# Kernel tuning notes

Measured on AMD Instinct MI355X. Metric: run time of the kernel, lower is better.

Reference implementation:

```python
import jax, jax.numpy as jnp
import numpy as np

DECAY = 0.999
EPS = 1e-05
COMMIT = 0.25


def _layer_norm(x, g, b, eps=1e-5):
    mu = x.mean(-1, keepdims=True)
    var = ((x - mu) ** 2).mean(-1, keepdims=True)
    return (x - mu) * jax.lax.rsqrt(var + eps) * g + b


def setup_inputs() -> dict:
    key = jax.random.key(0)
    ks = jax.random.split(key, 8)
    B, T, D, M, H = 8, 4096, 512, 1024, 512
    init_bound = 1.0 / 512
    embedding = jax.random.uniform(ks[0], (M, D), jnp.float32, -init_bound, init_bound)
    return {
        "dense_x": jax.random.normal(ks[1], (B, T, D), jnp.float32),
        "dense_padding_mask": jax.random.randint(ks[2], (B, T), 0, 2).astype(bool),
        "labels": jax.random.randint(ks[3], (B, T), 0, M),
        "embedding": embedding,
        "ema_count": jnp.zeros((M,), jnp.float32),
        "ema_weight": embedding,
        "ln1_g": jnp.ones((D,), jnp.float32),
        "ln1_b": jnp.zeros((D,), jnp.float32),
        "W1": jax.random.normal(ks[4], (D, H), jnp.float32) * (1.0 / np.sqrt(D)),
        "ln2_g": jnp.ones((H,), jnp.float32),
        "ln2_b": jnp.zeros((H,), jnp.float32),
        "W2": jax.random.normal(ks[5], (H, M), jnp.float32) * (1.0 / np.sqrt(H)),
    }


def reference(dense_x, dense_padding_mask, labels, embedding, ema_count, ema_weight,
              ln1_g, ln1_b, W1, ln2_g, ln2_b, W2):
    B, T, D = dense_x.shape
    M = embedding.shape[0]
    N = B * T

    # ---- VQ codebook (EMA) ----
    x_flat = jax.lax.stop_gradient(dense_x).reshape(N, D)
    distances = (jnp.sum(embedding ** 2, axis=1)[None, :]
                 + jnp.sum(x_flat ** 2, axis=1, keepdims=True)
                 - 2.0 * (x_flat @ embedding.T))
    indices = jnp.argmin(distances, axis=-1)  # [N]
    quantized = embedding[indices].reshape(B, T, D)

    # EMA codebook update (training path); encodings.sum(0) and encodings.T @ x
    # expressed as scatter-adds instead of materializing [N, M] one-hot.
    counts = jnp.zeros((M,), dense_x.dtype).at[indices].add(1.0)
    new_count = DECAY * ema_count + (1.0 - DECAY) * counts
    n = jnp.sum(new_count)
    new_count = (new_count + EPS) / (n + M * EPS) * n
    dw = jnp.zeros((M, D), dense_x.dtype).at[indices].add(x_flat)
    new_weight = DECAY * ema_weight + (1.0 - DECAY) * dw
    new_embedding = new_weight / new_count[:, None]

    e_latent_loss = (dense_x - jax.lax.stop_gradient(quantized)) ** 2  # [B,T,D]
    vq_loss = COMMIT * e_latent_loss
    quantized_st = dense_x + jax.lax.stop_gradient(quantized - dense_x)

    avg_probs = counts / N
    perplexity = jnp.exp(-jnp.sum(avg_probs * jnp.log(avg_probs + 1e-10)))

    # ---- decoder: LN -> ReLU -> Linear -> LN -> ReLU -> Linear ----
    h = jax.nn.relu(_layer_norm(dense_x, ln1_g, ln1_b)) @ W1      # [B,T,H]
    logits = jax.nn.relu(_layer_norm(h, ln2_g, ln2_b)) @ W2       # [B,T,M]

    # ---- cross-entropy with ignore_index=-1 (padding) ----
    lab = jnp.where(dense_padding_mask, -1, labels)
    valid = lab >= 0
    safe = jnp.where(valid, lab, 0)
    logp = jax.nn.log_softmax(logits, axis=-1)
    ce = -jnp.take_along_axis(logp, safe[..., None], axis=-1)[..., 0]
    recon_loss = jnp.where(valid, ce, 0.0)

    loss = recon_loss + vq_loss.sum(-1)  # [B,T]
    return quantized_st, loss, perplexity, new_embedding, new_count, new_weight
```

## Files before the change

kernel.cpp:

```cpp
#include <hip/hip_runtime.h>


#define N_TOK 32768
#define WAITV(n) __builtin_amdgcn_s_waitcnt(0x0F70 | (n))
#define BAR() __builtin_amdgcn_s_barrier()

typedef __attribute__((ext_vector_type(8))) short short8;
typedef _Float16 half8 __attribute__((ext_vector_type(8)));
typedef __attribute__((ext_vector_type(4))) float f32x4;

__device__ __forceinline__ f32x4 mfma16(short8 a, short8 b, f32x4 c) {
    return __builtin_amdgcn_mfma_f32_16x16x32_bf16(a, b, c, 0, 0, 0);
}
__device__ __forceinline__ f32x4 mfma16h(half8 a, half8 b, f32x4 c) {
    return __builtin_amdgcn_mfma_f32_16x16x32_f16(a, b, c, 0, 0, 0);
}

__device__ __forceinline__ void gl_lds16(const unsigned short* g, char* l) {
    __builtin_amdgcn_global_load_lds(
        (const __attribute__((address_space(1))) void*)g,
        (__attribute__((address_space(3))) void*)l, 16, 0, 0);
}

__device__ __forceinline__ unsigned short f2bf(float x) {
    unsigned u = __float_as_uint(x);
    u += 0x7fffu + ((u >> 16) & 1u);
    return (unsigned short)(u >> 16);
}
__device__ __forceinline__ float bf2f(unsigned short h) {
    return __uint_as_float(((unsigned)h) << 16);
}
__device__ __forceinline__ unsigned short f2h(float x) {
    union { _Float16 h; unsigned short u; } c;
    c.h = (_Float16)x;
    return c.u;
}
__device__ __forceinline__ float h2f(unsigned short u) {
    union { _Float16 h; unsigned short u; } c;
    c.u = u;
    return (float)c.h;
}

__device__ __forceinline__ float waveSum(float v) {
#pragma unroll
    for (int off = 32; off > 0; off >>= 1) v += __shfl_down(v, off, 64);
    return v;
}
__device__ __forceinline__ float xorSum(float v) {
#pragma unroll
    for (int off = 1; off < 64; off <<= 1) v += __shfl_xor(v, off);
    return v;
}

__global__ __launch_bounds__(256) void prep_x_kernel(
        const float* __restrict__ X, const float* __restrict__ g,
        const float* __restrict__ b, unsigned short* __restrict__ Xf,
        unsigned short* __restrict__ A1, unsigned long long* __restrict__ minpack) {
    int tid = threadIdx.x;
    if (tid < 4) minpack[(blockIdx.x << 2) + tid] = ~0ULL;
    int lane = tid & 63;
    int n = (blockIdx.x << 2) + (tid >> 6);
    const float* row = X + ((size_t)n << 9);
    float v[8]; float s = 0.f, ss = 0.f;
#pragma unroll
    for (int i = 0; i < 8; ++i) { v[i] = row[lane + (i << 6)]; s += v[i]; ss += v[i] * v[i]; }
    s = xorSum(s); ss = xorSum(ss);
    float mu = s * (1.f / 512.f);
    float rs = rsqrtf(ss * (1.f / 512.f) - mu * mu + 1e-5f);
#pragma unroll
    for (int i = 0; i < 8; ++i) {
        int c = lane + (i << 6);
        size_t o = ((size_t)n << 9) + c;
        float x = v[i];
        Xf[o] = f2h(x);
        float a = fmaxf((x - mu) * rs * g[c] + b[c], 0.f);
        A1[o] = f2bf(a);
    }
}

__global__ __launch_bounds__(256) void prep_e_kernel(
        const float* __restrict__ E, unsigned short* __restrict__ Ehf,
        unsigned short* __restrict__ Elf, float* __restrict__ e_sq,
        int* __restrict__ izero) {
    if (blockIdx.x < 8) izero[(blockIdx.x << 8) + threadIdx.x] = 0;
    int lane = threadIdx.x & 63;
    int m = (blockIdx.x << 2) + (threadIdx.x >> 6);
    const float* row = E + ((size_t)m << 9);
    float ss = 0.f;
#pragma unroll
    for (int i = 0; i < 8; ++i) {
        int c = lane + (i << 6);
        float x = row[c];
        ss += x * x;
        float xs = x * 512.f;
        unsigned short h = f2h(xs);
        size_t o = ((size_t)m << 9) + c;
        Ehf[o] = h;
        Elf[o] = f2h(xs - h2f(h));
    }
    ss = xorSum(ss);
    if (lane == 0) e_sq[m] = ss * 512.f;
}

__global__ __launch_bounds__(256) void prep_wt_kernel(
        const float* __restrict__ W1, const float* __restrict__ W2,
        unsigned short* __restrict__ W1T, unsigned short* __restrict__ W2T) {
    __shared__ float t[32][33];
    int bx = blockIdx.x;
    const float* W = (bx < 16) ? W1 : W2;
    unsigned short* WT = (bx < 16) ? W1T : W2T;
    int Nw = (bx < 16) ? 512 : 1024;
    int n0 = ((bx < 16) ? bx : (bx - 16)) << 5, k0 = blockIdx.y << 5;
    int tx = threadIdx.x & 31, ty = threadIdx.x >> 5;
#pragma unroll
    for (int l = 0; l < 4; ++l)
        t[ty + (l << 3)][tx] = W[(size_t)(k0 + ty + (l << 3)) * Nw + n0 + tx];
    __syncthreads();
#pragma unroll
    for (int l = 0; l < 4; ++l)
        WT[(((size_t)(n0 + ty + (l << 3))) << 9) + k0 + tx] = f2bf(t[tx][ty + (l << 3)]);
}

__device__ __forceinline__ unsigned long long packDist(float d, int m) {
    unsigned u = __float_as_uint(d);
    u = (u & 0x80000000u) ? ~u : (u | 0x80000000u);
    return ((unsigned long long)u << 32) | (unsigned)m;
}

__device__ __forceinline__ void dist_body(
        int q, int x, char* LB,
        const unsigned short* __restrict__ Xf,
        const unsigned short* __restrict__ Ehf, const unsigned short* __restrict__ Elf,
        const float* __restrict__ e_sq, unsigned long long* __restrict__ minpack) {
    int tid = threadIdx.x, lane = tid & 63, w = tid >> 6;
    int quad = lane >> 4, lanelo = lane & 15;
    int wm = w >> 1, wn = w & 1;
    int row0 = (((q >> 3) << 3) | x) << 7;
    int m0 = (q & 7) << 7;

    int srow = ((w & 1) << 6) + lane;
    int skoff = (w >> 1) << 4;
    const unsigned short* pX = Xf  + (((size_t)(row0 + srow)) << 9) + skoff;
    const unsigned short* pH = Ehf + (((size_t)(m0  + srow)) << 9) + skoff;
    const unsigned short* pL = Elf + (((size_t)(m0  + srow)) << 9) + skoff;
    char* ldsB = LB + ((w >> 1) << 12) + ((w & 1) << 10) + (lane << 4);
    const char* ra  = LB + (quad << 11) + (((wm << 6) + lanelo) << 4);
    const char* rbh = LB + 8192 + (quad << 11) + (((wn << 6) + lanelo) << 4);

    f32x4 acc[4][4];
#pragma unroll
    for (int i = 0; i < 4; ++i)
#pragma unroll
        for (int j = 0; j < 4; ++j) acc[i][j] = 0.f;

#pragma unroll
    for (int p = 0; p < 2; ++p) {
        char* d = ldsB + p * 24576;
        const unsigned short* sX = pX + (p << 5);
        const unsigned short* sH = pH + (p << 5);
        const unsigned short* sL = pL + (p << 5);
        gl_lds16(sX, d);            gl_lds16(sX + 8, d + 2048);
        gl_lds16(sH, d + 8192);     gl_lds16(sH + 8, d + 10240);
        gl_lds16(sL, d + 16384);    gl_lds16(sL + 8, d + 18432);
    }

#pragma unroll
    for (int it = 0; it < 16; ++it) {
        const int cb = it % 3;
        if (it < 14) {
            const int nb = (it + 2) % 3;
            const unsigned short* sX = pX + ((it + 2) << 5);
            const unsigned short* sH = pH + ((it + 2) << 5);
            const unsigned short* sL = pL + ((it + 2) << 5);
            char* d = ldsB + nb * 24576;
            gl_lds16(sX, d);            gl_lds16(sX + 8, d + 2048);
            gl_lds16(sH, d + 8192);     gl_lds16(sH + 8, d + 10240);
            gl_lds16(sL, d + 16384);    gl_lds16(sL + 8, d + 18432);
            WAITV(12);
        } else if (it == 14) {
            WAITV(6);
        } else {
            WAITV(0);
        }
        BAR();
        const char* A  = ra  + cb * 24576;
        const char* Bh = rbh + cb * 24576;
        half8 av[4], bh[4], bl[4];
#pragma unroll
        for (int i = 0; i < 4; ++i) av[i] = *(const half8*)(A + (i << 8));
#pragma unroll
        for (int j = 0; j < 4; ++j) {
            bh[j] = *(const half8*)(Bh + (j << 8));
            bl[j] = *(const half8*)(Bh + 8192 + (j << 8));
        }
#pragma unroll
        for (int i = 0; i < 4; ++i)
#pragma unroll
            for (int j = 0; j < 4; ++j) acc[i][j] = mfma16h(av[i], bh[j], acc[i][j]);
#pragma unroll
        for (int i = 0; i < 4; ++i)
#pragma unroll
            for (int j = 0; j < 4; ++j) acc[i][j] = mfma16h(av[i], bl[j], acc[i][j]);
        BAR();
    }

    float esq[4];
#pragma unroll
    for (int j = 0; j < 4; ++j) esq[j] = e_sq[m0 + (wn << 6) + (j << 4) + lanelo];
#pragma unroll
    for (int i = 0; i < 4; ++i)
#pragma unroll
        for (int r = 0; r < 4; ++r) {
            unsigned long long best = ~0ULL;
#pragma unroll
            for (int j = 0; j < 4; ++j) {
                int code = m0 + (wn << 6) + (j << 4) + lanelo;
                float d = esq[j] - 2.f * acc[i][j][r];
                unsigned long long p = packDist(d, code);
                if (p < best) best = p;
            }
#pragma unroll
            for (int off = 1; off < 16; off <<= 1) {
                unsigned long long q2 = __shfl_xor(best, off);
                if (q2 < best) best = q2;
            }
            if (lanelo == 0) {
                int t = row0 + (wm << 6) + (i << 4) + (quad << 2) + r;
                atomicMin(&minpack[t], best);
            }
        }
}

__device__ __forceinline__ void gemm_core(
        char* LB, const unsigned short* pA, const unsigned short* pB,
        int w, int lane, int quad, int lanelo, int wm, int wn,
        f32x4 (*acc)[4], bool bf) {
    char* ldsB = LB + ((w >> 1) << 12) + ((w & 1) << 10) + (lane << 4);
    const char* ra = LB + (quad << 11) + (((wm << 6) + lanelo) << 4);
    const char* rb = LB + 8192 + (quad << 11) + (((wn << 6) + lanelo) << 4);

#pragma unroll
    for (int p = 0; p < 2; ++p) {
        char* d = ldsB + p * 16384;
        const unsigned short* sA = pA + (p << 5);
        const unsigned short* sB = pB + (p << 5);
        gl_lds16(sA, d);            gl_lds16(sA + 8, d + 2048);
        gl_lds16(sB, d + 8192);     gl_lds16(sB + 8, d + 10240);
    }

#pragma unroll
    for (int it = 0; it < 16; ++it) {
        const int cb = it % 3;
        if (it < 14) {
            const int nb = (it + 2) % 3;
            const unsigned short* sA = pA + ((it + 2) << 5);
            const unsigned short* sB = pB + ((it + 2) << 5);
            char* d = ldsB + nb * 16384;
            gl_lds16(sA, d);            gl_lds16(sA + 8, d + 2048);
            gl_lds16(sB, d + 8192);     gl_lds16(sB + 8, d + 10240);
            WAITV(8);
        } else if (it == 14) {
            WAITV(4);
        } else {
            WAITV(0);
        }
        BAR();
        const char* A = ra + cb * 16384;
        const char* B = rb + cb * 16384;
        short8 af[4], bf4[4];
#pragma unroll
        for (int i = 0; i < 4; ++i) af[i] = *(const short8*)(A + (i << 8));
#pragma unroll
        for (int j = 0; j < 4; ++j) bf4[j] = *(const short8*)(B + (j << 8));
#pragma unroll
        for (int i = 0; i < 4; ++i)
#pragma unroll
            for (int j = 0; j < 4; ++j) acc[i][j] = mfma16(af[i], bf4[j], acc[i][j]);
        BAR();
    }
    (void)bf;
}

__device__ __forceinline__ void gemm1_body(
        int g, int x, char* LB,
        const unsigned short* __restrict__ A1, const unsigned short* __restrict__ W1T,
        unsigned short* __restrict__ Hb) {
    int tid = threadIdx.x, lane = tid & 63, w = tid >> 6;
    int quad = lane >> 4, lanelo = lane & 15;
    int wm = w >> 1, wn = w & 1;
    int row0 = (((g >> 2) << 3) | x) << 7;
    int n0 = (g & 3) << 7;

    int srow = ((w & 1) << 6) + lane;
    int skoff = (w >> 1) << 4;
    const unsigned short* pA = A1  + (((size_t)(row0 + srow)) << 9) + skoff;
    const unsigned short* pB = W1T + (((size_t)(n0   + srow)) << 9) + skoff;

    f32x4 acc[4][4];
#pragma unroll
    for (int i = 0; i < 4; ++i)
#pragma unroll
        for (int j = 0; j < 4; ++j) acc[i][j] = 0.f;

    gemm_core(LB, pA, pB, w, lane, quad, lanelo, wm, wn, acc, true);

#pragma unroll
    for (int i = 0; i < 4; ++i)
#pragma unroll
        for (int j = 0; j < 4; ++j)
#pragma unroll
            for (int r = 0; r < 4; ++r) {
                int row = row0 + (wm << 6) + (i << 4) + (quad << 2) + r;
                int col = n0 + (wn << 6) + (j << 4) + lanelo;
                Hb[((size_t)row << 9) + col] = f2bf(acc[i][j][r]);
            }
}

__global__ __launch_bounds__(256) void fused1_kernel(
        const unsigned short* __restrict__ Xf,
        const unsigned short* __restrict__ Ehf, const unsigned short* __restrict__ Elf,
        const float* __restrict__ e_sq, unsigned long long* __restrict__ minpack,
        const unsigned short* __restrict__ A1, const unsigned short* __restrict__ W1T,
        unsigned short* __restrict__ Hb) {
    __shared__ __align__(16) char LB[73728];
    int b = blockIdx.x, x = b & 7, m = b >> 3;
    int t = m % 3, g = m / 3;
    if (t < 2) dist_body((g << 1) + t, x, LB, Xf, Ehf, Elf, e_sq, minpack);
    else       gemm1_body(g, x, LB, A1, W1T, Hb);
}

__global__ __launch_bounds__(256) void fused2_kernel(
        const float* __restrict__ X, const float* __restrict__ E,
        const unsigned long long* __restrict__ minpack,
        float* __restrict__ out_q, int* __restrict__ icounts,
        float* __restrict__ vqsum,
        const unsigned short* __restrict__ Hb, const float* __restrict__ g2,
        const float* __restrict__ b2, unsigned short* __restrict__ A2) {
    int nb = blockIdx.x >> 1;
    int lane = threadIdx.x & 63;
    int n = (nb << 2) + (threadIdx.x >> 6);
    if ((blockIdx.x & 1) == 0) {
        int idx = (int)(minpack[n] & 0xFFFFFFFFULL);
        if (lane == 0) atomicAdd(&icounts[idx], 1);
        const float* xr = X + ((size_t)n << 9);
        const float* er = E + ((size_t)idx << 9);
        float s = 0.f;
#pragma unroll
        for (int i = 0; i < 8; ++i) {
            int c = lane + (i << 6);
            float xv = xr[c], q = er[c];
            out_q[((size_t)n << 9) + c] = q;
            float dlt = xv - q;
            s += dlt * dlt;
        }
        s = waveSum(s);
        if (lane == 0) vqsum[n] = 0.25f * s;
    } else {
        const unsigned short* row = Hb + ((size_t)n << 9);
        float v[8]; float s = 0.f, ss = 0.f;
#pragma unroll
        for (int i = 0; i < 8; ++i) { v[i] = bf2f(row[lane + (i << 6)]); s += v[i]; ss += v[i] * v[i]; }
        s = xorSum(s); ss = xorSum(ss);
        float mu = s * (1.f / 512.f);
        float rs = rsqrtf(ss * (1.f / 512.f) - mu * mu + 1e-5f);
#pragma unroll
        for (int i = 0; i < 8; ++i) {
            int c = lane + (i << 6);
            float a = fmaxf((v[i] - mu) * rs * g2[c] + b2[c], 0.f);
            A2[((size_t)n << 9) + c] = f2bf(a);
        }
    }
}

__global__ __launch_bounds__(1024) void codebook_kernel(
        const float* __restrict__ ema_count, const int* __restrict__ icounts,
        float* __restrict__ out_perp, float* __restrict__ out_newcount,
        int* __restrict__ offsets) {
    __shared__ int sc[1024];
    __shared__ float red[16];
    int tid = threadIdx.x;
    int lane = tid & 63, wid = tid >> 6;
    int ic = icounts[tid];
    sc[tid] = ic;
    for (int off = 1; off < 1024; off <<= 1) {
        __syncthreads();
        int v = (tid >= off) ? sc[tid - off] : 0;
        __syncthreads();
        sc[tid] += v;
    }
    offsets[tid] = sc[tid] - ic;
    __syncthreads();

    float cnt = (float)ic;
    float raw = 0.999f * ema_count[tid] + 0.001f * cnt;
    float v = waveSum(raw);
    if (lane == 0) red[wid] = v;
    __syncthreads();
    float nsum = 0.f;
#pragma unroll
    for (int i = 0; i < 16; ++i) nsum += red[i];
    __syncthreads();
    float p = cnt * (1.f / 32768.f);
    float e = p * logf(p + 1e-10f);
    e = waveSum(e);
    if (lane == 0) red[wid] = e;
    __syncthreads();
    float ent = 0.f;
#pragma unroll
    for (int i = 0; i < 16; ++i) ent += red[i];
    float nc = (raw + 1e-5f) / (nsum + 1024.f * 1e-5f) * nsum;
    out_newcount[tid] = nc;
    if (tid == 0) out_perp[0] = expf(-ent);
}

__global__ __launch_bounds__(256) void scatter_kernel(
        const unsigned long long* __restrict__ minpack,
        const int* __restrict__ offsets, int* __restrict__ cursor,
        int* __restrict__ bucket) {
    int n = (blockIdx.x << 8) + threadIdx.x;
    int idx = (int)(minpack[n] & 0xFFFFFFFFULL);
    int pos = atomicAdd(&cursor[idx], 1);
    bucket[offsets[idx] + pos] = n;
}

__device__ __forceinline__ void dw_body(
        int m, char* LB, const float* __restrict__ X,
        const int* __restrict__ bucket, const int* __restrict__ icounts,
        const int* __restrict__ offsets, float* __restrict__ dw) {
    float* comb = (float*)LB;
    int tid = threadIdx.x, lane = tid & 63, w = tid >> 6;
    int cnt = icounts[m], base = offsets[m];
    float acc[8] = {};
    for (int i = w; i < cnt; i += 4) {
        int t = bucket[base + i];
        const float* xr = X + ((size_t)t << 9);
#pragma unroll
        for (int j = 0; j < 8; ++j) acc[j] += xr[lane + (j << 6)];
    }
#pragma unroll
    for (int j = 0; j < 8; ++j) comb[(w << 9) + lane + (j << 6)] = acc[j];
    __syncthreads();
    for (int c = tid; c < 512; c += 256)
        dw[((size_t)m << 9) + c] = comb[c] + comb[512 + c] + comb[1024 + c] + comb[1536 + c];
}

__device__ __forceinline__ void gemm2_body(
        int q, int x, char* LB,
        float (*lmax)[2][64], float (*lsum)[2][64], float* llab, int* slab,
        const unsigned short* __restrict__ A2, const unsigned short* __restrict__ W2T,
        const int* __restrict__ mask, const int* __restrict__ labels,
        float* __restrict__ ws_cmax, float* __restrict__ ws_csum,
        float* __restrict__ ws_lab) {
    int tid = threadIdx.x, lane = tid & 63, w = tid >> 6;
    int quad = lane >> 4, lanelo = lane & 15;
    int wm = w >> 1, wn = w & 1;
    int row0 = (((q >> 3) << 3) | x) << 7;
    int cy = q & 7;
    int c0 = cy << 7;
    if (tid < 128) {
        int mk = mask[row0 + tid];
        slab[tid] = mk ? 0 : labels[row0 + tid];
    }
    __syncthreads();

    int srow = ((w & 1) << 6) + lane;
    int skoff = (w >> 1) << 4;
    const unsigned short* pA = A2  + (((size_t)(row0 + srow)) << 9) + skoff;
    const unsigned short* pB = W2T + (((size_t)(c0   + srow)) << 9) + skoff;

    f32x4 acc[4][4];
#pragma unroll
    for (int i = 0; i < 4; ++i)
#pragma unroll
        for (int j = 0; j < 4; ++j) acc[i][j] = 0.f;

    gemm_core(LB, pA, pB, w, lane, quad, lanelo, wm, wn, acc, true);

#pragma unroll
    for (int i = 0; i < 4; ++i)
#pragma unroll
        for (int j = 0; j < 4; ++j)
#pragma unroll
            for (int r = 0; r < 4; ++r) {
                int code = c0 + (wn << 6) + (j << 4) + lanelo;
                int tt = (wm << 6) + (i << 4) + (quad << 2) + r;
                if (code == slab[tt]) llab[tt] = acc[i][j][r];
            }
#pragma unroll
    for (int i = 0; i < 4; ++i)
#pragma unroll
        for (int r = 0; r < 4; ++r) {
            float mx = fmaxf(fmaxf(acc[i][0][r], acc[i][1][r]),
                             fmaxf(acc[i][2][r], acc[i][3][r]));
#pragma unroll
            for (int off = 1; off < 16; off <<= 1) mx = fmaxf(mx, __shfl_xor(mx, off));
            if (lanelo == 0) lmax[wm][wn][(i << 4) + (quad << 2) + r] = mx;
        }
    __syncthreads();
#pragma unroll
    for (int i = 0; i < 4; ++i)
#pragma unroll
        for (int r = 0; r < 4; ++r) {
            int tl = (i << 4) + (quad << 2) + r;
            float cm = fmaxf(lmax[wm][0][tl], lmax[wm][1][tl]);
            float s2 = expf(acc[i][0][r] - cm) + expf(acc[i][1][r] - cm) +
                       expf(acc[i][2][r] - cm) + expf(acc[i][3][r] - cm);
#pragma unroll
            for (int off = 1; off < 16; off <<= 1) s2 += __shfl_xor(s2, off);
            if (lanelo == 0) lsum[wm][wn][tl] = s2;
        }
    __syncthreads();
    if (tid < 128) {
        int wmi = tid >> 6, tl = tid & 63;
        int token = row0 + tid;
        float cm = fmaxf(lmax[wmi][0][tl], lmax[wmi][1][tl]);
        float cs = lsum[wmi][0][tl] + lsum[wmi][1][tl];
        size_t o = ((size_t)cy << 15) + token;
        ws_cmax[o] = cm;
        ws_csum[o] = cs;
        if ((slab[tid] >> 7) == cy) ws_lab[token] = llab[tid];
    }
}

__global__ __launch_bounds__(256) void fused3_kernel(
        const unsigned short* __restrict__ A2, const unsigned short* __restrict__ W2T,
        const int* __restrict__ mask, const int* __restrict__ labels,
        float* __restrict__ ws_cmax, float* __restrict__ ws_csum,
        float* __restrict__ ws_lab,
        const float* __restrict__ X, const int* __restrict__ bucket,
        const int* __restrict__ icounts, const int* __restrict__ offsets,
        float* __restrict__ dw) {
    __shared__ __align__(16) char LB[49152];
    __shared__ float lmax[2][2][64], lsum[2][2][64], llab[128];
    __shared__ int slab[128];
    int b = blockIdx.x, x = b & 7, m = b >> 3;
    int t = m % 3, g = m / 3;
    if (t < 2) gemm2_body((g << 1) + t, x, LB, lmax, lsum, llab, slab,
                          A2, W2T, mask, labels, ws_cmax, ws_csum, ws_lab);
    else       dw_body((g << 3) | x, LB, X, bucket, icounts, offsets, dw);
}

__global__ __launch_bounds__(256) void epilogue_kernel(
        const float* __restrict__ ema_weight, const float* __restrict__ dw,
        const float* __restrict__ newcount, float* __restrict__ out_neww,
        float* __restrict__ out_newemb,
        const float* __restrict__ ws_cmax, const float* __restrict__ ws_csum,
        const float* __restrict__ ws_lab, const int* __restrict__ mask,
        const float* __restrict__ vqsum, float* __restrict__ loss_out) {
    int bx = blockIdx.x;
    if (bx < 2048) {
        int i = (bx << 8) + threadIdx.x;
        float nw = 0.999f * ema_weight[i] + 0.001f * dw[i];
        out_neww[i] = nw;
        out_newemb[i] = nw / newcount[i >> 9];
    } else {
        int n = ((bx - 2048) << 8) + threadIdx.x;
        float m[8], s[8];
#pragma unroll
        for (int c = 0; c < 8; ++c) {
            m[c] = ws_cmax[(c << 15) + n];
            s[c] = ws_csum[(c << 15) + n];
        }
        float gm = m[0];
#pragma unroll
        for (int c = 1; c < 8; ++c) gm = fmaxf(gm, m[c]);
        float se = 0.f;
#pragma unroll
        for (int c = 0; c < 8; ++c) se += s[c] * expf(m[c] - gm);
        float ce = -(ws_lab[n] - gm - logf(se));
        loss_out[n] = (mask[n] ? 0.f : ce) + vqsum[n];
    }
}

extern "C" void kernel_launch(void* const* d_in, const int* in_sizes, int n_in,
                              void* d_out, int out_size, void* d_ws, size_t ws_size,
                              hipStream_t stream) {
    const float* X          = (const float*)d_in[0];
    const int*   mask       = (const int*)d_in[1];
    const int*   labels     = (const int*)d_in[2];
    const float* E          = (const float*)d_in[3];
    const float* ema_count  = (const float*)d_in[4];
    const float* ema_weight = (const float*)d_in[5];
    const float* g1 = (const float*)d_in[6];
    const float* b1 = (const float*)d_in[7];
    const float* W1 = (const float*)d_in[8];
    const float* g2 = (const float*)d_in[9];
    const float* b2 = (const float*)d_in[10];
    const float* W2 = (const float*)d_in[11];

    float* out = (float*)d_out;
    float* out_q        = out;
    float* out_loss     = out + 16777216;
    float* out_perp     = out + 16809984;
    float* out_newemb   = out + 16809985;
    float* out_newcount = out + 17334273;
    float* out_neww     = out + 17335297;

    float* w = (float*)d_ws;
    float* vqsum = w;  w += 32768;
    float* e_sq = w;   w += 1024;
    float* dwbuf = w;  w += 524288;
    unsigned long long* minpack = (unsigned long long*)w; w += 65536;
    float* ws_cmax = w; w += 262144;
    float* ws_csum = w; w += 262144;
    float* ws_lab  = w; w += 32768;
    int* icounts = (int*)w; w += 1024;
    int* cursor  = (int*)w; w += 1024;
    int* offsets = (int*)w; w += 1024;
    int* bucket  = (int*)w; w += 32768;
    unsigned short* Ehf = (unsigned short*)w; w += 262144;
    unsigned short* Elf = (unsigned short*)w; w += 262144;
    unsigned short* W1T = (unsigned short*)w; w += 131072;
    unsigned short* W2T = (unsigned short*)w; w += 262144;
    unsigned short* Xf  = (unsigned short*)w; w += 8388608;
    unsigned short* A1  = (unsigned short*)w; w += 8388608;
    unsigned short* Hb  = (unsigned short*)w; w += 8388608;
    unsigned short* A2  = Xf;

    prep_e_kernel<<<256, 256, 0, stream>>>(E, Ehf, Elf, e_sq, icounts);
    prep_wt_kernel<<<dim3(48, 16), 256, 0, stream>>>(W1, W2, W1T, W2T);
    prep_x_kernel<<<8192, 256, 0, stream>>>(X, g1, b1, Xf, A1, minpack);
    fused1_kernel<<<3072, 256, 0, stream>>>(Xf, Ehf, Elf, e_sq, minpack,
                                            A1, W1T, Hb);
    fused2_kernel<<<16384, 256, 0, stream>>>(X, E, minpack, out_q, icounts,
                                             vqsum, Hb, g2, b2, A2);
    codebook_kernel<<<1, 1024, 0, stream>>>(ema_count, icounts, out_perp,
                                            out_newcount, offsets);
    scatter_kernel<<<128, 256, 0, stream>>>(minpack, offsets, cursor, bucket);
    fused3_kernel<<<3072, 256, 0, stream>>>(A2, W2T, mask, labels,
                                            ws_cmax, ws_csum, ws_lab,
                                            X, bucket, icounts, offsets, dwbuf);
    epilogue_kernel<<<2176, 256, 0, stream>>>(ema_weight, dwbuf, out_newcount,
                                              out_neww, out_newemb,
                                              ws_cmax, ws_csum, ws_lab,
                                              mask, vqsum, out_loss);
}
```

Baseline: 481.4 us.

## Enlarge GEMM tiles to 256 rows with 512-thread blocks and double buffering

The distance, GEMM1 and GEMM2 bodies now use 512-thread blocks, each covering 256 token rows instead of 128, so every codebook or weight tile loaded into LDS is reused across twice as many rows. The three-stage LDS ring becomes two-stage double buffering to fit the larger tiles, and grids are halved to match. The dw body is widened to use eight waves, and the fused3 block mapping changes so GEMM2 and dw blocks alternate. The trade-offs are a shallower prefetch pipeline, higher LDS use per block and fewer resident blocks, which may expose more memory latency.

```diff
diff --git a/kernel.cpp b/kernel.cpp
--- a/kernel.cpp
+++ b/kernel.cpp
@@ -135,17 +135,18 @@
     int tid = threadIdx.x, lane = tid & 63, w = tid >> 6;
     int quad = lane >> 4, lanelo = lane & 15;
     int wm = w >> 1, wn = w & 1;
-    int row0 = (((q >> 3) << 3) | x) << 7;
+    int row0 = (((q >> 3) << 3) | x) << 8;
     int m0 = (q & 7) << 7;
 
-    int srow = ((w & 1) << 6) + lane;
-    int skoff = (w >> 1) << 4;
-    const unsigned short* pX = Xf  + (((size_t)(row0 + srow)) << 9) + skoff;
-    const unsigned short* pH = Ehf + (((size_t)(m0  + srow)) << 9) + skoff;
-    const unsigned short* pL = Elf + (((size_t)(m0  + srow)) << 9) + skoff;
-    char* ldsB = LB + ((w >> 1) << 12) + ((w & 1) << 10) + (lane << 4);
-    const char* ra  = LB + (quad << 11) + (((wm << 6) + lanelo) << 4);
-    const char* rbh = LB + 8192 + (quad << 11) + (((wn << 6) + lanelo) << 4);
+    int mA = tid & 255, kA = tid >> 8;
+    int nB = tid & 127, kB = tid >> 7;
+    const unsigned short* pA = Xf  + (((size_t)(row0 + mA)) << 9) + (kA << 3);
+    const unsigned short* pH = Ehf + (((size_t)(m0  + nB)) << 9) + (kB << 3);
+    const unsigned short* pL = Elf + (((size_t)(m0  + nB)) << 9) + (kB << 3);
+    char* dA = LB + (tid << 4);
+    char* dB = LB + 16384 + (tid << 4);
+    const char* ra  = LB + (quad << 12) + (((wm << 6) + lanelo) << 4);
+    const char* rbh = LB + 16384 + (quad << 11) + (((wn << 6) + lanelo) << 4);
 
     f32x4 acc[4][4];
 #pragma unroll
@@ -153,38 +154,27 @@
 #pragma unroll
         for (int j = 0; j < 4; ++j) acc[i][j] = 0.f;
 
-#pragma unroll
-    for (int p = 0; p < 2; ++p) {
-        char* d = ldsB + p * 24576;
-        const unsigned short* sX = pX + (p << 5);
-        const unsigned short* sH = pH + (p << 5);
-        const unsigned short* sL = pL + (p << 5);
-        gl_lds16(sX, d);            gl_lds16(sX + 8, d + 2048);
-        gl_lds16(sH, d + 8192);     gl_lds16(sH + 8, d + 10240);
-        gl_lds16(sL, d + 16384);    gl_lds16(sL + 8, d + 18432);
-    }
+    gl_lds16(pA, dA);   gl_lds16(pA + 16, dA + 8192);
+    gl_lds16(pH, dB);   gl_lds16(pL, dB + 8192);
 
 #pragma unroll
     for (int it = 0; it < 16; ++it) {
-        const int cb = it % 3;
-        if (it < 14) {
-            const int nb = (it + 2) % 3;
-            const unsigned short* sX = pX + ((it + 2) << 5);
-            const unsigned short* sH = pH + ((it + 2) << 5);
-            const unsigned short* sL = pL + ((it + 2) << 5);
-            char* d = ldsB + nb * 24576;
-            gl_lds16(sX, d);            gl_lds16(sX + 8, d + 2048);
-            gl_lds16(sH, d + 8192);     gl_lds16(sH + 8, d + 10240);
-            gl_lds16(sL, d + 16384);    gl_lds16(sL + 8, d + 18432);
-            WAITV(12);
-        } else if (it == 14) {
-            WAITV(6);
+        const int cb = it & 1;
+        if (it < 15) {
+            const unsigned short* sA = pA + ((it + 1) << 5);
+            const unsigned short* sH = pH + ((it + 1) << 5);
+            const unsigned short* sL = pL + ((it + 1) << 5);
+            char* eA = dA + (cb ^ 1) * 32768;
+            char* eB = dB + (cb ^ 1) * 32768;
+            gl_lds16(sA, eA);   gl_lds16(sA + 16, eA + 8192);
+            gl_lds16(sH, eB);   gl_lds16(sL, eB + 8192);
+            WAITV(4);
         } else {
             WAITV(0);
         }
         BAR();
-        const char* A  = ra  + cb * 24576;
-        const char* Bh = rbh + cb * 24576;
+        const char* A  = ra  + cb * 32768;
+        const char* Bh = rbh + cb * 32768;
         half8 av[4], bh[4], bl[4];
 #pragma unroll
         for (int i = 0; i < 4; ++i) av[i] = *(const half8*)(A + (i << 8));
@@ -231,42 +221,37 @@
         }
 }
 
-__device__ __forceinline__ void gemm_core(
+__device__ __forceinline__ void gemm_core512(
         char* LB, const unsigned short* pA, const unsigned short* pB,
-        int w, int lane, int quad, int lanelo, int wm, int wn,
-        f32x4 (*acc)[4], bool bf) {
-    char* ldsB = LB + ((w >> 1) << 12) + ((w & 1) << 10) + (lane << 4);
-    const char* ra = LB + (quad << 11) + (((wm << 6) + lanelo) << 4);
-    const char* rb = LB + 8192 + (quad << 11) + (((wn << 6) + lanelo) << 4);
-
-#pragma unroll
-    for (int p = 0; p < 2; ++p) {
-        char* d = ldsB + p * 16384;
-        const unsigned short* sA = pA + (p << 5);
-        const unsigned short* sB = pB + (p << 5);
-        gl_lds16(sA, d);            gl_lds16(sA + 8, d + 2048);
-        gl_lds16(sB, d + 8192);     gl_lds16(sB + 8, d + 10240);
-    }
+        f32x4 (*acc)[4]) {
+    int tid = threadIdx.x, lane = tid & 63, w = tid >> 6;
+    int quad = lane >> 4, lanelo = lane & 15;
+    int wm = w >> 1, wn = w & 1;
+    char* dA = LB + (tid << 4);
+    char* dB = LB + 16384 + (tid << 4);
+    const char* ra = LB + (quad << 12) + (((wm << 6) + lanelo) << 4);
+    const char* rb = LB + 16384 + (quad << 11) + (((wn << 6) + lanelo) << 4);
+
+    gl_lds16(pA, dA);   gl_lds16(pA + 16, dA + 8192);
+    gl_lds16(pB, dB);
 
 #pragma unroll
     for (int it = 0; it < 16; ++it) {
-        const int cb = it % 3;
-        if (it < 14) {
-            const int nb = (it + 2) % 3;
-            const unsigned short* sA = pA + ((it + 2) << 5);
-            const unsigned short* sB = pB + ((it + 2) << 5);
-            char* d = ldsB + nb * 16384;
-            gl_lds16(sA, d);            gl_lds16(sA + 8, d + 2048);
-            gl_lds16(sB, d + 8192);     gl_lds16(sB + 8, d + 10240);
-            WAITV(8);
-        } else if (it == 14) {
-            WAITV(4);
+        const int cb = it & 1;
+        if (it < 15) {
+            const unsigned short* sA = pA + ((it + 1) << 5);
+            const unsigned short* sB = pB + ((it + 1) << 5);
+            char* eA = dA + (cb ^ 1) * 24576;
+            char* eB = dB + (cb ^ 1) * 24576;
+            gl_lds16(sA, eA);   gl_lds16(sA + 16, eA + 8192);
+            gl_lds16(sB, eB);
+            WAITV(3);
         } else {
             WAITV(0);
         }
         BAR();
-        const char* A = ra + cb * 16384;
-        const char* B = rb + cb * 16384;
+        const char* A = ra + cb * 24576;
+        const char* B = rb + cb * 24576;
         short8 af[4], bf4[4];
 #pragma unroll
         for (int i = 0; i < 4; ++i) af[i] = *(const short8*)(A + (i << 8));
@@ -278,7 +263,6 @@
             for (int j = 0; j < 4; ++j) acc[i][j] = mfma16(af[i], bf4[j], acc[i][j]);
         BAR();
     }
-    (void)bf;
 }
 
 __device__ __forceinline__ void gemm1_body(
@@ -288,13 +272,13 @@
     int tid = threadIdx.x, lane = tid & 63, w = tid >> 6;
     int quad = lane >> 4, lanelo = lane & 15;
     int wm = w >> 1, wn = w & 1;
-    int row0 = (((g >> 2) << 3) | x) << 7;
+    int row0 = (((g >> 2) << 3) | x) << 8;
     int n0 = (g & 3) << 7;
 
-    int srow = ((w & 1) << 6) + lane;
-    int skoff = (w >> 1) << 4;
-    const unsigned short* pA = A1  + (((size_t)(row0 + srow)) << 9) + skoff;
-    const unsigned short* pB = W1T + (((size_t)(n0   + srow)) << 9) + skoff;
+    int mA = tid & 255, kA = tid >> 8;
+    int nB = tid & 127, kB = tid >> 7;
+    const unsigned short* pA = A1  + (((size_t)(row0 + mA)) << 9) + (kA << 3);
+    const unsigned short* pB = W1T + (((size_t)(n0   + nB)) << 9) + (kB << 3);
 
     f32x4 acc[4][4];
 #pragma unroll
@@ -302,7 +286,7 @@
 #pragma unroll
         for (int j = 0; j < 4; ++j) acc[i][j] = 0.f;
 
-    gemm_core(LB, pA, pB, w, lane, quad, lanelo, wm, wn, acc, true);
+    gemm_core512(LB, pA, pB, acc);
 
 #pragma unroll
     for (int i = 0; i < 4; ++i)
@@ -316,13 +300,13 @@
             }
 }
 
-__global__ __launch_bounds__(256) void fused1_kernel(
+__global__ __launch_bounds__(512) void fused1_kernel(
         const unsigned short* __restrict__ Xf,
         const unsigned short* __restrict__ Ehf, const unsigned short* __restrict__ Elf,
         const float* __restrict__ e_sq, unsigned long long* __restrict__ minpack,
         const unsigned short* __restrict__ A1, const unsigned short* __restrict__ W1T,
         unsigned short* __restrict__ Hb) {
-    __shared__ __align__(16) char LB[73728];
+    __shared__ __align__(16) char LB[65536];
     int b = blockIdx.x, x = b & 7, m = b >> 3;
     int t = m % 3, g = m / 3;
     if (t < 2) dist_body((g << 1) + t, x, LB, Xf, Ehf, Elf, e_sq, minpack);
@@ -431,7 +415,7 @@
     int tid = threadIdx.x, lane = tid & 63, w = tid >> 6;
     int cnt = icounts[m], base = offsets[m];
     float acc[8] = {};
-    for (int i = w; i < cnt; i += 4) {
+    for (int i = w; i < cnt; i += 8) {
         int t = bucket[base + i];
         const float* xr = X + ((size_t)t << 9);
 #pragma unroll
@@ -440,8 +424,13 @@
 #pragma unroll
     for (int j = 0; j < 8; ++j) comb[(w << 9) + lane + (j << 6)] = acc[j];
     __syncthreads();
-    for (int c = tid; c < 512; c += 256)
-        dw[((size_t)m << 9) + c] = comb[c] + comb[512 + c] + comb[1024 + c] + comb[1536 + c];
+    int c = tid;
+    if (c < 512) {
+        float s = 0.f;
+#pragma unroll
+        for (int p = 0; p < 8; ++p) s += comb[(p << 9) + c];
+        dw[((size_t)m << 9) + c] = s;
+    }
 }
 
 __device__ __forceinline__ void gemm2_body(
@@ -454,19 +443,19 @@
     int tid = threadIdx.x, lane = tid & 63, w = tid >> 6;
     int quad = lane >> 4, lanelo = lane & 15;
     int wm = w >> 1, wn = w & 1;
-    int row0 = (((q >> 3) << 3) | x) << 7;
+    int row0 = (((q >> 3) << 3) | x) << 8;
     int cy = q & 7;
     int c0 = cy << 7;
-    if (tid < 128) {
+    if (tid < 256) {
         int mk = mask[row0 + tid];
         slab[tid] = mk ? 0 : labels[row0 + tid];
     }
     __syncthreads();
 
-    int srow = ((w & 1) << 6) + lane;
-    int skoff = (w >> 1) << 4;
-    const unsigned short* pA = A2  + (((size_t)(row0 + srow)) << 9) + skoff;
-    const unsigned short* pB = W2T + (((size_t)(c0   + srow)) << 9) + skoff;
+    int mA = tid & 255, kA = tid >> 8;
+    int nB = tid & 127, kB = tid >> 7;
+    const unsigned short* pA = A2  + (((size_t)(row0 + mA)) << 9) + (kA << 3);
+    const unsigned short* pB = W2T + (((size_t)(c0   + nB)) << 9) + (kB << 3);
 
     f32x4 acc[4][4];
 #pragma unroll
@@ -474,7 +463,7 @@
 #pragma unroll
         for (int j = 0; j < 4; ++j) acc[i][j] = 0.f;
 
-    gemm_core(LB, pA, pB, w, lane, quad, lanelo, wm, wn, acc, true);
+    gemm_core512(LB, pA, pB, acc);
 
 #pragma unroll
     for (int i = 0; i < 4; ++i)
@@ -510,7 +499,7 @@
             if (lanelo == 0) lsum[wm][wn][tl] = s2;
         }
     __syncthreads();
-    if (tid < 128) {
+    if (tid < 256) {
         int wmi = tid >> 6, tl = tid & 63;
         int token = row0 + tid;
         float cm = fmaxf(lmax[wmi][0][tl], lmax[wmi][1][tl]);
@@ -522,7 +511,7 @@
     }
 }
 
-__global__ __launch_bounds__(256) void fused3_kernel(
+__global__ __launch_bounds__(512) void fused3_kernel(
         const unsigned short* __restrict__ A2, const unsigned short* __restrict__ W2T,
         const int* __restrict__ mask, const int* __restrict__ labels,
         float* __restrict__ ws_cmax, float* __restrict__ ws_csum,
@@ -531,13 +520,13 @@
         const int* __restrict__ icounts, const int* __restrict__ offsets,
         float* __restrict__ dw) {
     __shared__ __align__(16) char LB[49152];
-    __shared__ float lmax[2][2][64], lsum[2][2][64], llab[128];
-    __shared__ int slab[128];
+    __shared__ float lmax[4][2][64], lsum[4][2][64], llab[256];
+    __shared__ int slab[256];
     int b = blockIdx.x, x = b & 7, m = b >> 3;
-    int t = m % 3, g = m / 3;
-    if (t < 2) gemm2_body((g << 1) + t, x, LB, lmax, lsum, llab, slab,
-                          A2, W2T, mask, labels, ws_cmax, ws_csum, ws_lab);
-    else       dw_body((g << 3) | x, LB, X, bucket, icounts, offsets, dw);
+    int t = m & 1, g = m >> 1;
+    if (t == 0) gemm2_body(g, x, LB, lmax, lsum, llab, slab,
+                           A2, W2T, mask, labels, ws_cmax, ws_csum, ws_lab);
+    else        dw_body((g << 3) | x, LB, X, bucket, icounts, offsets, dw);
 }
 
 __global__ __launch_bounds__(256) void epilogue_kernel(
@@ -620,14 +609,14 @@
     prep_e_kernel<<<256, 256, 0, stream>>>(E, Ehf, Elf, e_sq, icounts);
     prep_wt_kernel<<<dim3(48, 16), 256, 0, stream>>>(W1, W2, W1T, W2T);
     prep_x_kernel<<<8192, 256, 0, stream>>>(X, g1, b1, Xf, A1, minpack);
-    fused1_kernel<<<3072, 256, 0, stream>>>(Xf, Ehf, Elf, e_sq, minpack,
+    fused1_kernel<<<1536, 512, 0, stream>>>(Xf, Ehf, Elf, e_sq, minpack,
                                             A1, W1T, Hb);
     fused2_kernel<<<16384, 256, 0, stream>>>(X, E, minpack, out_q, icounts,
                                              vqsum, Hb, g2, b2, A2);
     codebook_kernel<<<1, 1024, 0, stream>>>(ema_count, icounts, out_perp,
                                             out_newcount, offsets);
     scatter_kernel<<<128, 256, 0, stream>>>(minpack, offsets, cursor, bucket);
-    fused3_kernel<<<3072, 256, 0, stream>>>(A2, W2T, mask, labels,
+    fused3_kernel<<<2048, 512, 0, stream>>>(A2, W2T, mask, labels,
                                             ws_cmax, ws_csum, ws_lab,
                                             X, bucket, icounts, offsets, dwbuf);
     epilogue_kernel<<<2176, 256, 0, stream>>>(ema_weight, dwbuf, out_newcount,
```

Result: no change. 486.7 us (+1.1%).
